# Kernel optimization log

Hardware: AMD Instinct MI355X
Metric: run time of the kernel (lower is better)

## Reference

```python
import jax, jax.numpy as jnp
import numpy as np

N = 4096          # n_neurons
M = 10            # max_memory
T = 10            # max_ticks
B = 1024          # batch
P = N // 2 // 2   # n_pairs = 1024
AD = 64           # attention_dim


def ln(x, g, b, eps=1e-5):
    m = x.mean(-1, keepdims=True)
    v = ((x - m) ** 2).mean(-1, keepdims=True)
    return (x - m) * jax.lax.rsqrt(v + eps) * g + b


def setup_inputs() -> dict:
    key = jax.random.key(0)
    ks = iter(jax.random.split(key, 64))

    def rn(shape, s=0.05):
        return (jax.random.normal(next(ks), shape) * s).astype(jnp.float32)

    d = {}
    d['x'] = jax.random.normal(next(ks), (B, 1, 28, 28), dtype=jnp.float32)
    d['post0'] = jax.random.normal(next(ks), (N, M), dtype=jnp.float32)
    d['pre0'] = jax.random.normal(next(ks), (N, M), dtype=jnp.float32)
    d['pairs'] = jax.random.randint(next(ks), (P, 2), 0, N)
    d['decay'] = jnp.full((P,), 0.1, jnp.float32)
    # image encoder: 784 -> 128 -> 32 -> 4
    d['ie_w1'] = rn((784, 128)); d['ie_b1'] = jnp.zeros(128); d['ie_g1'] = jnp.ones(128); d['ie_be1'] = jnp.zeros(128)
    d['ie_w2'] = rn((128, 32));  d['ie_b2'] = jnp.zeros(32);  d['ie_g2'] = jnp.ones(32);  d['ie_be2'] = jnp.zeros(32)
    d['ie_w3'] = rn((32, 4));    d['ie_b3'] = jnp.zeros(4)
    # synapse model: (4+N) -> 256 -> N
    d['sy_w1'] = rn((4 + N, 256)); d['sy_b1'] = jnp.zeros(256); d['sy_g'] = jnp.ones(256); d['sy_be'] = jnp.zeros(256)
    d['sy_w2'] = rn((256, N));     d['sy_b2'] = jnp.zeros(N)
    # batched per-neuron models: M -> 128 -> 1
    d['nm_w1'] = rn((N, M, 128)); d['nm_b1'] = jnp.zeros((N, 128))
    d['nm_g'] = jnp.ones((N, 128)); d['nm_be'] = jnp.zeros((N, 128))
    d['nm_w2'] = rn((N, 128));    d['nm_b2'] = jnp.zeros(N)
    # attention projections
    d['key_w'] = rn((4, AD)); d['key_b'] = jnp.zeros(AD)
    d['val_w'] = rn((4, AD)); d['val_b'] = jnp.zeros(AD)
    d['q_w'] = rn((P, AD));   d['q_b'] = jnp.zeros(AD)
    # syncronization reader: (AD+P) -> 512 -> 64 -> 10
    d['rd_w1'] = rn((AD + P, 512)); d['rd_b1'] = jnp.zeros(512); d['rd_g1'] = jnp.ones(512); d['rd_be1'] = jnp.zeros(512)
    d['rd_w2'] = rn((512, 64));     d['rd_b2'] = jnp.zeros(64);  d['rd_g2'] = jnp.ones(64);  d['rd_be2'] = jnp.zeros(64)
    d['rd_w3'] = rn((64, 10));      d['rd_b3'] = jnp.zeros(10)
    return d


def reference(x, post0, pre0, pairs, decay,
              ie_w1, ie_b1, ie_g1, ie_be1, ie_w2, ie_b2, ie_g2, ie_be2, ie_w3, ie_b3,
              sy_w1, sy_b1, sy_g, sy_be, sy_w2, sy_b2,
              nm_w1, nm_b1, nm_g, nm_be, nm_w2, nm_b2,
              key_w, key_b, val_w, val_b, q_w, q_b,
              rd_w1, rd_b1, rd_g1, rd_be1, rd_w2, rd_b2, rd_g2, rd_be2, rd_w3, rd_b3):
    b = x.shape[0]
    fx = x.reshape(b, -1)
    # image encoder
    e = jax.nn.relu(ln(fx @ ie_w1 + ie_b1, ie_g1, ie_be1))
    e = jax.nn.relu(ln(e @ ie_w2 + ie_b2, ie_g2, ie_be2))
    enc = e @ ie_w3 + ie_b3                               # [B,4]
    keys = enc @ key_w + key_b                            # [B,AD]
    values = enc @ val_w + val_b                          # [B,AD]
    post, pre = post0, pre0
    pred = None
    for tick in range(T):
        last_post = jnp.broadcast_to(post[:, -1][None, :], (b, N))
        syn_in = jnp.concatenate([enc, last_post], axis=1)            # [B,4+N]
        h = jax.nn.relu(ln(syn_in @ sy_w1 + sy_b1, sy_g, sy_be))
        new_pre = h @ sy_w2 + sy_b2                                   # [B,N]
        pre = jnp.concatenate([pre[:, 1:], new_pre.mean(0)[:, None]], axis=1)
        # batched per-neuron MLP over history
        h2 = jax.nn.relu(ln(jnp.einsum('nm,nmh->nh', pre, nm_w1) + nm_b1, nm_g, nm_be))
        new_post = jnp.einsum('nh,nh->n', h2, nm_w2) + nm_b2          # [N]
        post = jnp.concatenate([post[:, 1:], new_post[:, None]], axis=1)
        # decayed pair synchronization
        L = min(tick + 1, M)
        Zi = post[pairs[:, 0], M - L:]                                # [P,L]
        Zj = post[pairs[:, 1], M - L:]
        td = jnp.arange(L - 1, -1, -1, dtype=post.dtype)              # [L]
        R = jnp.exp(-decay[:, None] * td[None, :])                    # [P,L]
        sync = jnp.sum(Zi * R * Zj, axis=1) / (jnp.sum(R, axis=1) + 1e-8)  # [P]
        sv = jnp.broadcast_to(sync[None, :], (b, P))                  # [B,P]
        q = sv @ q_w + q_b                                            # [B,AD]
        scores = jnp.sum(q * keys, axis=-1, keepdims=True) / jnp.sqrt(jnp.float32(AD))
        aw = jax.nn.softmax(scores, axis=-1)                          # [B,1] -> ones
        att = aw * values                                             # [B,AD]
        comb = jnp.concatenate([att, sv], axis=-1)                    # [B,AD+P]
        r = jax.nn.relu(ln(comb @ rd_w1 + rd_b1, rd_g1, rd_be1))
        r = jax.nn.relu(ln(r @ rd_w2 + rd_b2, rd_g2, rd_be2))
        pred = r @ rd_w3 + rd_b3                                      # [B,10]
    return pred
```

## Files before the change

### kernel.cpp

```cpp
#include <hip/hip_runtime.h>

#define N_ 4096
#define M_ 10
#define T_ 10
#define B_ 1024
#define P_ 1024
#define NBLK 256
#define NTHR 512

__device__ __forceinline__ float wave_red_sum(float v) {
#pragma unroll
  for (int m = 32; m >= 1; m >>= 1) v += __shfl_xor(v, m);
  return v;
}

__device__ __forceinline__ float gld(const float* p) {
  return __hip_atomic_load(p, __ATOMIC_RELAXED, __HIP_MEMORY_SCOPE_AGENT);
}
__device__ __forceinline__ void gst(float* p, float v) {
  __hip_atomic_store(p, v, __ATOMIC_RELAXED, __HIP_MEMORY_SCOPE_AGENT);
}

__device__ __forceinline__ void gridbar(unsigned* bar, unsigned bar_no, int g) {
  asm volatile("s_waitcnt vmcnt(0)" ::: "memory");
  __syncthreads();
  if (threadIdx.x == 0) {
    __hip_atomic_fetch_add(&bar[(g & 7) * 32], 1u, __ATOMIC_RELAXED, __HIP_MEMORY_SCOPE_AGENT);
    if (g == 0) {
      const unsigned target = bar_no * (NBLK / 8);
      bool done;
      do {
        done = true;
#pragma unroll
        for (int i = 0; i < 8; ++i)
          done &= (__hip_atomic_load(&bar[i * 32], __ATOMIC_RELAXED, __HIP_MEMORY_SCOPE_AGENT) >= target);
        if (!done) __builtin_amdgcn_s_sleep(1);
      } while (!done);
#pragma unroll
      for (int i = 0; i < 8; ++i)
        __hip_atomic_store(&bar[256 + i * 32], bar_no, __ATOMIC_RELAXED, __HIP_MEMORY_SCOPE_AGENT);
    } else {
      unsigned* mygen = &bar[256 + (g & 7) * 32];
      while (__hip_atomic_load(mygen, __ATOMIC_RELAXED, __HIP_MEMORY_SCOPE_AGENT) < bar_no)
        __builtin_amdgcn_s_sleep(1);
    }
  }
  asm volatile("" ::: "memory");
  __syncthreads();
}

__global__ void k_init(unsigned* __restrict__ bar) {
  if (threadIdx.x < 512)
    __hip_atomic_store(bar + threadIdx.x, 0u, __ATOMIC_RELAXED, __HIP_MEMORY_SCOPE_AGENT);
}

struct MArgs {
  const float *x, *post0, *pre0;
  const int* pairs;
  const float* decay;
  const float *iew1, *ieb1, *ieg1, *iebe1, *iew2, *ieb2, *ieg2, *iebe2, *iew3, *ieb3;
  const float *syw1, *syb1, *syg, *sybe, *syw2, *syb2;
  const float *nw1, *nb1, *ng, *nbe, *nw2, *nb2;
  const float *vw, *vb;
  const float *rdw1, *rdb1, *rdg1, *rdbe1, *rdw2, *rdb2, *rdg2, *rdbe2, *rdw3, *rdb3;
  float *pc, *pc2, *enc_g, *hbar, *postG, *syncv, *scp;
  float* out;
  unsigned* bar;
};

__global__ __launch_bounds__(NTHR)
void k_mega(MArgs a) {
  const int g = blockIdx.x, tid = threadIdx.x;
  const int lane = tid & 63;
  const int n0 = g * 16;
  const int b0e = g * 4;

  __shared__ float s_w1[16 * M_ * 128];
  __shared__ float s_syw1[16 * 256];
  __shared__ float s_w4[4 * 256];
  __shared__ float scratch[6144];
  __shared__ float s_post[16][M_];
  __shared__ float s_pre[16][M_];
  __shared__ float s_pl[16];
  __shared__ float s_hbar[256];
  __shared__ float s_cval[256];
  __shared__ float s_tmp[2][256];
  __shared__ float s_red[16];
  __shared__ float s_values[4][64];
  __shared__ float s_stat[6];
  __shared__ float s_mw[4];
  __shared__ float s_mww[16];

  unsigned bar_no = 0;

  {
    const float4* src = (const float4*)(a.nw1 + n0 * M_ * 128);
    float4* dst = (float4*)s_w1;
    for (int i = tid; i < 16 * M_ * 128 / 4; i += NTHR) dst[i] = src[i];
    const float4* s2 = (const float4*)(a.syw1 + (4 + n0) * 256);
    float4* d2 = (float4*)s_syw1;
    for (int i = tid; i < 16 * 256 / 4; i += NTHR) d2[i] = s2[i];
    const float4* s3 = (const float4*)a.syw1;
    float4* d3 = (float4*)s_w4;
    for (int i = tid; i < 1024 / 4; i += NTHR) d3[i] = s3[i];
    if (tid < 160) {
      int r = tid / 10, m = tid - r * 10;
      s_post[r][m] = a.post0[(n0 + r) * M_ + m];
      s_pre[r][m]  = a.pre0[(n0 + r) * M_ + m];
    }
    float* fx = scratch;
    for (int i = tid; i < 4 * 784; i += NTHR) fx[i] = a.x[b0e * 784 + i];
  }
  __syncthreads();
  if (tid < 16) s_pl[tid] = s_post[tid][M_ - 1];

  {
    float* fx = scratch;
    float* e1 = scratch + 3200;
    int r = tid >> 7, j = tid & 127;
    float u = a.ieb1[j];
    const float* fxr = fx + r * 784;
    for (int k = 0; k < 784; ++k) u += fxr[k] * a.iew1[k * 128 + j];
    float s = wave_red_sum(u), sq = wave_red_sum(u * u);
    int w = tid >> 6;
    if (lane == 0) { s_tmp[0][w] = s; s_tmp[1][w] = sq; }
    __syncthreads();
    float S = s_tmp[0][r * 2] + s_tmp[0][r * 2 + 1];
    float S2 = s_tmp[1][r * 2] + s_tmp[1][r * 2 + 1];
    float mm = S * (1.f / 128.f), vv = S2 * (1.f / 128.f) - mm * mm;
    e1[r * 128 + j] = fmaxf((u - mm) * rsqrtf(vv + 1e-5f) * a.ieg1[j] + a.iebe1[j], 0.f);
  }
  __syncthreads();
  {
    float* e1 = scratch + 3200;
    float* e2 = scratch + 3712;
    if (tid < 128) {
      int r = tid >> 5, jj = tid & 31;
      float u = a.ieb2[jj];
      for (int k = 0; k < 128; ++k) u += e1[r * 128 + k] * a.iew2[k * 32 + jj];
      float ss = u, sq = u * u;
#pragma unroll
      for (int m = 16; m >= 1; m >>= 1) { ss += __shfl_xor(ss, m, 32); sq += __shfl_xor(sq, m, 32); }
      float mm = ss * (1.f / 32.f), vv = sq * (1.f / 32.f) - mm * mm;
      e2[r * 32 + jj] = fmaxf((u - mm) * rsqrtf(vv + 1e-5f) * a.ieg2[jj] + a.iebe2[jj], 0.f);
    }
  }
  __syncthreads();
  {
    float* e2 = scratch + 3712;
    float* encs = scratch + 3840;
    if (tid < 16) {
      int r = tid >> 2, o = tid & 3;
      float u = a.ieb3[o];
      for (int k = 0; k < 32; ++k) u += e2[r * 32 + k] * a.iew3[k * 4 + o];
      encs[r * 4 + o] = u;
      gst(&a.enc_g[(b0e + r) * 4 + o], u);
    }
    __syncthreads();
    if (tid < 256) {
      int r = tid >> 6, v = tid & 63;
      float u = a.vb[v];
#pragma unroll
      for (int o = 0; o < 4; ++o) u += encs[r * 4 + o] * a.vw[o * 64 + v];
      s_values[r][v] = u;
    }
  }
  __syncthreads();
  {
    int j = tid & 255, half = tid >> 8;
    float acc = 0.f;
#pragma unroll
    for (int r = 0; r < 8; ++r) {
      int n = half * 8 + r;
      acc += s_pl[n] * s_syw1[n * 256 + j];
    }
    s_tmp[half][j] = acc;
  }
  __syncthreads();
  if (tid < 256) gst(&a.pc[g * 256 + tid], s_tmp[0][tid] + s_tmp[1][tid]);
  ++bar_no; gridbar(a.bar, bar_no, g);

  for (int t = 0; t < T_; ++t) {
    if (g < 8) {
      int j = tid & 255, half = tid >> 8;
      float acc = 0.f;
#pragma unroll 4
      for (int r = 0; r < 16; ++r)
        acc += gld(&a.pc[(g * 32 + half * 16 + r) * 256 + j]);
      s_tmp[half][j] = acc;
      __syncthreads();
      if (tid < 256) gst(&a.pc2[g * 256 + tid], s_tmp[0][tid] + s_tmp[1][tid]);
    }
    ++bar_no; gridbar(a.bar, bar_no, g);

    if (g < 64) {
      float* encT = scratch;
      float* mb = scratch + 4096;
      float* rb = scratch + 5120;
      if (t == 0) {
        for (int i = tid; i < 4096; i += NTHR) {
          int b = i >> 2, o = i & 3;
          encT[o * 1024 + b] = gld(&a.enc_g[i]);
        }
        float q[14];
        if (tid < 256) {
          float w0 = s_w4[tid], w1v = s_w4[256 + tid], w2v = s_w4[512 + tid], w3v = s_w4[768 + tid];
          float wv[4] = {w0, w1v, w2v, w3v};
          int idx = 0;
#pragma unroll
          for (int o = 0; o < 4; ++o) q[idx++] = wv[o];
#pragma unroll
          for (int o = 0; o < 4; ++o)
#pragma unroll
            for (int p = 0; p <= o; ++p) q[idx++] = wv[o] * wv[p];
        } else {
#pragma unroll
          for (int i = 0; i < 14; ++i) q[i] = 0.f;
        }
#pragma unroll
        for (int i = 0; i < 14; ++i) q[i] = wave_red_sum(q[i]);
        if (lane == 0) {
          int w = tid >> 6;
#pragma unroll
          for (int i = 0; i < 14; ++i) s_tmp[1][w * 16 + i] = q[i];
        }
        __syncthreads();
        if (tid < 14) {
          float S = 0.f;
#pragma unroll
          for (int w = 0; w < 8; ++w) S += s_tmp[1][w * 16 + tid];
          s_red[tid] = S * (1.f / 256.f);
        }
        __syncthreads();
        if (tid < 4) s_mw[tid] = s_red[tid];
        if (tid < 16) {
          int o = tid >> 2, p = tid & 3;
          int hi = o > p ? o : p, lo = o > p ? p : o;
          s_mww[tid] = s_red[4 + hi * (hi + 1) / 2 + lo];
        }
        __syncthreads();
      }
      if (tid < 256) {
        float acc = a.syb1[tid];
#pragma unroll
        for (int s = 0; s < 8; ++s) acc += gld(&a.pc2[s * 256 + tid]);
        s_cval[tid] = acc;
      }
      __syncthreads();
      {
        float p[6];
        if (tid < 256) {
          float c = s_cval[tid];
          p[0] = c; p[1] = c * c;
          p[2] = c * s_w4[tid];
          p[3] = c * s_w4[256 + tid];
          p[4] = c * s_w4[512 + tid];
          p[5] = c * s_w4[768 + tid];
        } else {
#pragma unroll
          for (int i = 0; i < 6; ++i) p[i] = 0.f;
        }
#pragma unroll
        for (int i = 0; i < 6; ++i) p[i] = wave_red_sum(p[i]);
        if (lane == 0) {
          int w = tid >> 6;
#pragma unroll
          for (int i = 0; i < 6; ++i) s_tmp[0][w * 8 + i] = p[i];
        }
        __syncthreads();
        if (tid < 6) {
          float S = 0.f;
#pragma unroll
          for (int w = 0; w < 8; ++w) S += s_tmp[0][w * 8 + tid];
          s_stat[tid] = S * (1.f / 256.f);
        }
        __syncthreads();
      }
      for (int b = tid; b < 1024; b += NTHR) {
        float e0 = encT[b], e1v = encT[1024 + b], e2v = encT[2048 + b], e3v = encT[3072 + b];
        float m = s_stat[0] + e0 * s_mw[0] + e1v * s_mw[1] + e2v * s_mw[2] + e3v * s_mw[3];
        float eu2 = s_stat[1] + 2.f * (e0 * s_stat[2] + e1v * s_stat[3] + e2v * s_stat[4] + e3v * s_stat[5]);
        float ee[4] = {e0, e1v, e2v, e3v};
        float qf = 0.f;
#pragma unroll
        for (int o = 0; o < 4; ++o)
#pragma unroll
          for (int p = 0; p < 4; ++p) qf += ee[o] * ee[p] * s_mww[o * 4 + p];
        eu2 += qf;
        mb[b] = m;
        rb[b] = rsqrtf(eu2 - m * m + 1e-5f);
      }
      __syncthreads();
      {
        int jj = 4 * g + (tid >> 7);
        int bt = tid & 127;
        float cj = s_cval[jj];
        float w0 = s_w4[jj], w1v = s_w4[256 + jj], w2v = s_w4[512 + jj], w3v = s_w4[768 + jj];
        float gj = a.syg[jj], bj = a.sybe[jj];
        float acc = 0.f;
#pragma unroll
        for (int bb = 0; bb < 8; ++bb) {
          int b = bb * 128 + bt;
          float u = cj + encT[b] * w0 + encT[1024 + b] * w1v + encT[2048 + b] * w2v + encT[3072 + b] * w3v;
          float y = (u - mb[b]) * rb[b] * gj + bj;
          acc += fmaxf(y, 0.f);
        }
        acc = wave_red_sum(acc);
        int w = tid >> 6;
        if (lane == 0) s_tmp[0][w] = acc;
        __syncthreads();
        if ((tid & 127) == 0)
          gst(&a.hbar[jj], (s_tmp[0][w] + s_tmp[0][w + 1]) * (1.f / 1024.f));
      }
    }
    ++bar_no; gridbar(a.bar, bar_no, g);

    {
      if (tid < 256) s_hbar[tid] = gld(&a.hbar[tid]);
      __syncthreads();
      {
        int nl = tid & 15, kq = tid >> 4;
        float u = 0.f;
#pragma unroll
        for (int kk = 0; kk < 8; ++kk) {
          int k = kq * 8 + kk;
          u += s_hbar[k] * a.syw2[k * N_ + n0 + nl];
        }
        ((float*)s_tmp)[kq * 16 + nl] = u;
      }
      __syncthreads();
      if (tid < 16) {
        float v = a.syb2[n0 + tid];
#pragma unroll
        for (int q = 0; q < 32; ++q) v += ((float*)s_tmp)[q * 16 + tid];
#pragma unroll
        for (int m = 0; m < M_ - 1; ++m) s_pre[tid][m] = s_pre[tid][m + 1];
        s_pre[tid][M_ - 1] = v;
      }
      __syncthreads();
      {
        int grp = tid >> 7, jj = tid & 127;
        int wv = tid >> 6;
#pragma unroll
        for (int rd = 0; rd < 4; ++rd) {
          int nl = rd * 4 + grp;
          int n2 = n0 + nl;
          float u = a.nb1[n2 * 128 + jj];
#pragma unroll
          for (int m = 0; m < M_; ++m) u += s_pre[nl][m] * s_w1[(nl * M_ + m) * 128 + jj];
          float s = wave_red_sum(u), sq = wave_red_sum(u * u);
          if (lane == 0) { s_red[wv * 2] = s; s_red[wv * 2 + 1] = sq; }
          __syncthreads();
          float S = s_red[grp * 4 + 0] + s_red[grp * 4 + 2];
          float S2 = s_red[grp * 4 + 1] + s_red[grp * 4 + 3];
          float mm = S * (1.f / 128.f), vv = S2 * (1.f / 128.f) - mm * mm;
          float y = fmaxf((u - mm) * rsqrtf(vv + 1e-5f) * a.ng[n2 * 128 + jj] + a.nbe[n2 * 128 + jj], 0.f);
          float d = wave_red_sum(y * a.nw2[n2 * 128 + jj]);
          __syncthreads();
          if (lane == 0) s_red[wv] = d;
          __syncthreads();
          if (jj == 0) {
            float npost = s_red[grp * 2] + s_red[grp * 2 + 1] + a.nb2[n2];
#pragma unroll
            for (int m = 0; m < M_ - 1; ++m) s_post[nl][m] = s_post[nl][m + 1];
            s_post[nl][M_ - 1] = npost;
            s_pl[nl] = npost;
          }
          __syncthreads();
        }
      }
      if (t < T_ - 1) {
        int j = tid & 255, half = tid >> 8;
        float acc = 0.f;
#pragma unroll
        for (int r = 0; r < 8; ++r) {
          int n = half * 8 + r;
          acc += s_pl[n] * s_syw1[n * 256 + j];
        }
        s_tmp[half][j] = acc;
        __syncthreads();
        if (tid < 256) gst(&a.pc[g * 256 + tid], s_tmp[0][tid] + s_tmp[1][tid]);
      } else {
        if (tid < 160) {
          int r = tid / 10, m = tid - r * 10;
          gst(&a.postG[(n0 + r) * M_ + m], s_post[r][m]);
        }
      }
    }
    ++bar_no; gridbar(a.bar, bar_no, g);
  }

  if (tid < 4) {
    int p = g * 4 + tid;
    int i = a.pairs[p * 2], jn = a.pairs[p * 2 + 1];
    float dc = a.decay[p];
    float num = 0.f, den = 0.f;
#pragma unroll
    for (int l = 0; l < M_; ++l) {
      float r = expf(-dc * (float)(M_ - 1 - l));
      num += gld(&a.postG[i * M_ + l]) * r * gld(&a.postG[jn * M_ + l]);
      den += r;
    }
    gst(&a.syncv[p], num / (den + 1e-8f));
  }
  ++bar_no; gridbar(a.bar, bar_no, g);

  if (g < 8) {
    if (tid < 128) s_tmp[0][tid] = gld(&a.syncv[g * 128 + tid]);
    __syncthreads();
    float acc = 0.f;
    for (int i = 0; i < 128; ++i)
      acc += s_tmp[0][i] * a.rdw1[(64 + g * 128 + i) * 512 + tid];
    gst(&a.scp[g * 512 + tid], acc);
  }
  ++bar_no; gridbar(a.bar, bar_no, g);

  {
    float* r1 = scratch;
    float* r2 = scratch + 2048;
    float* red = scratch + 2304;
    float* p2 = scratch + 2368;
    float base = a.rdb1[tid];
#pragma unroll
    for (int s = 0; s < 8; ++s) base += gld(&a.scp[s * 512 + tid]);
    float u[4];
#pragma unroll
    for (int r = 0; r < 4; ++r) u[r] = base;
    for (int k = 0; k < 64; ++k) {
      float w = a.rdw1[k * 512 + tid];
#pragma unroll
      for (int r = 0; r < 4; ++r) u[r] += s_values[r][k] * w;
    }
    int wid = tid >> 6;
#pragma unroll
    for (int r = 0; r < 4; ++r) {
      float s = wave_red_sum(u[r]), sq = wave_red_sum(u[r] * u[r]);
      if (lane == 0) { red[r * 16 + wid * 2] = s; red[r * 16 + wid * 2 + 1] = sq; }
    }
    __syncthreads();
    float gg = a.rdg1[tid], bb = a.rdbe1[tid];
#pragma unroll
    for (int r = 0; r < 4; ++r) {
      float S = 0.f, S2 = 0.f;
#pragma unroll
      for (int w = 0; w < 8; ++w) { S += red[r * 16 + w * 2]; S2 += red[r * 16 + w * 2 + 1]; }
      float m = S * (1.f / 512.f), v = S2 * (1.f / 512.f) - m * m;
      r1[r * 512 + tid] = fmaxf((u[r] - m) * rsqrtf(v + 1e-5f) * gg + bb, 0.f);
    }
    __syncthreads();
    int o = tid & 63, kq = tid >> 6;
    float u2[4] = {0.f, 0.f, 0.f, 0.f};
#pragma unroll
    for (int kk = 0; kk < 64; ++kk) {
      int k = kq * 64 + kk;
      float w = a.rdw2[k * 64 + o];
#pragma unroll
      for (int r = 0; r < 4; ++r) u2[r] += r1[r * 512 + k] * w;
    }
#pragma unroll
    for (int r = 0; r < 4; ++r) p2[(kq * 4 + r) * 64 + o] = u2[r];
    __syncthreads();
    if (tid < 256) {
      int r = tid >> 6, o2 = tid & 63;
      float v = a.rdb2[o2];
#pragma unroll
      for (int q = 0; q < 8; ++q) v += p2[(q * 4 + r) * 64 + o2];
      float s = wave_red_sum(v), sq = wave_red_sum(v * v);
      float m = s * (1.f / 64.f), var = sq * (1.f / 64.f) - m * m;
      r2[r * 64 + o2] = fmaxf((v - m) * rsqrtf(var + 1e-5f) * a.rdg2[o2] + a.rdbe2[o2], 0.f);
    }
    __syncthreads();
    if (tid < 40) {
      int r = tid / 10, o3 = tid - r * 10;
      float acc = a.rdb3[o3];
#pragma unroll
      for (int k = 0; k < 64; ++k) acc += r2[r * 64 + k] * a.rdw3[k * 10 + o3];
      a.out[(b0e + r) * 10 + o3] = acc;
    }
  }
}

extern "C" void kernel_launch(void* const* d_in, const int* in_sizes, int n_in,
                              void* d_out, int out_size, void* d_ws, size_t ws_size,
                              hipStream_t stream) {
  MArgs a;
  a.x     = (const float*)d_in[0];
  a.post0 = (const float*)d_in[1];
  a.pre0  = (const float*)d_in[2];
  a.pairs = (const int*)d_in[3];
  a.decay = (const float*)d_in[4];
  a.iew1  = (const float*)d_in[5];
  a.ieb1  = (const float*)d_in[6];
  a.ieg1  = (const float*)d_in[7];
  a.iebe1 = (const float*)d_in[8];
  a.iew2  = (const float*)d_in[9];
  a.ieb2  = (const float*)d_in[10];
  a.ieg2  = (const float*)d_in[11];
  a.iebe2 = (const float*)d_in[12];
  a.iew3  = (const float*)d_in[13];
  a.ieb3  = (const float*)d_in[14];
  a.syw1  = (const float*)d_in[15];
  a.syb1  = (const float*)d_in[16];
  a.syg   = (const float*)d_in[17];
  a.sybe  = (const float*)d_in[18];
  a.syw2  = (const float*)d_in[19];
  a.syb2  = (const float*)d_in[20];
  a.nw1   = (const float*)d_in[21];
  a.nb1   = (const float*)d_in[22];
  a.ng    = (const float*)d_in[23];
  a.nbe   = (const float*)d_in[24];
  a.nw2   = (const float*)d_in[25];
  a.nb2   = (const float*)d_in[26];
  a.vw    = (const float*)d_in[29];
  a.vb    = (const float*)d_in[30];
  a.rdw1  = (const float*)d_in[33];
  a.rdb1  = (const float*)d_in[34];
  a.rdg1  = (const float*)d_in[35];
  a.rdbe1 = (const float*)d_in[36];
  a.rdw2  = (const float*)d_in[37];
  a.rdb2  = (const float*)d_in[38];
  a.rdg2  = (const float*)d_in[39];
  a.rdbe2 = (const float*)d_in[40];
  a.rdw3  = (const float*)d_in[41];
  a.rdb3  = (const float*)d_in[42];
  a.out = (float*)d_out;

  float* ws = (float*)d_ws;
  a.pc    = ws;
  a.pc2   = ws + 65536;
  a.enc_g = ws + 67584;
  a.hbar  = ws + 71680;
  a.postG = ws + 71936;
  a.syncv = ws + 112896;
  a.scp   = ws + 113920;
  a.bar   = (unsigned*)(ws + 118016);

  k_init<<<1, 512, 0, stream>>>(a.bar);
  k_mega<<<NBLK, NTHR, 0, stream>>>(a);
}
```

Before: 212.5 us.

## Replace grid barriers with targeted counters and flags between producer/consumer block subsets

Replaces the full grid barrier (one master block polling, then broadcasting) with monotonic arrival counters and flags. Each stage now waits only for the blocks that produce its inputs: 8 reducer blocks wait on all 256, block 0 waits on the reducers, 64 blocks wait on block 0's flag, and everyone waits on those 64. Block 0 now computes the shared column statistics once and publishes them, instead of all 64 blocks recomputing them. The per-neuron MLP loop is also restructured to process 16 neurons in parallel with 32-lane shuffles instead of 4 serial rounds with block syncs. The cost is more intricate ordering logic and an extra serialized hop through block 0.

```diff
diff --git a/kernel.cpp b/kernel.cpp
--- a/kernel.cpp
+++ b/kernel.cpp
@@ -20,37 +20,39 @@
 __device__ __forceinline__ void gst(float* p, float v) {
   __hip_atomic_store(p, v, __ATOMIC_RELAXED, __HIP_MEMORY_SCOPE_AGENT);
 }
-
-__device__ __forceinline__ void gridbar(unsigned* bar, unsigned bar_no, int g) {
+__device__ __forceinline__ unsigned ld_u(unsigned* p) {
+  return __hip_atomic_load(p, __ATOMIC_RELAXED, __HIP_MEMORY_SCOPE_AGENT);
+}
+
+__device__ __forceinline__ void drain_sync() {
   asm volatile("s_waitcnt vmcnt(0)" ::: "memory");
   __syncthreads();
+}
+__device__ __forceinline__ void arrive8(unsigned* line8, int g) {
+  if (threadIdx.x == 0)
+    __hip_atomic_fetch_add(&line8[(g & 7) * 32], 1u, __ATOMIC_RELAXED, __HIP_MEMORY_SCOPE_AGENT);
+}
+__device__ __forceinline__ void wait_sum8(unsigned* line8, unsigned target) {
   if (threadIdx.x == 0) {
-    __hip_atomic_fetch_add(&bar[(g & 7) * 32], 1u, __ATOMIC_RELAXED, __HIP_MEMORY_SCOPE_AGENT);
-    if (g == 0) {
-      const unsigned target = bar_no * (NBLK / 8);
-      bool done;
-      do {
-        done = true;
-#pragma unroll
-        for (int i = 0; i < 8; ++i)
-          done &= (__hip_atomic_load(&bar[i * 32], __ATOMIC_RELAXED, __HIP_MEMORY_SCOPE_AGENT) >= target);
-        if (!done) __builtin_amdgcn_s_sleep(1);
-      } while (!done);
-#pragma unroll
-      for (int i = 0; i < 8; ++i)
-        __hip_atomic_store(&bar[256 + i * 32], bar_no, __ATOMIC_RELAXED, __HIP_MEMORY_SCOPE_AGENT);
-    } else {
-      unsigned* mygen = &bar[256 + (g & 7) * 32];
-      while (__hip_atomic_load(mygen, __ATOMIC_RELAXED, __HIP_MEMORY_SCOPE_AGENT) < bar_no)
-        __builtin_amdgcn_s_sleep(1);
-    }
-  }
-  asm volatile("" ::: "memory");
+    unsigned s;
+    do {
+      s = 0;
+#pragma unroll
+      for (int i = 0; i < 8; ++i) s += ld_u(&line8[i * 32]);
+      if (s < target) __builtin_amdgcn_s_sleep(1);
+    } while (s < target);
+  }
+  __syncthreads();
+}
+__device__ __forceinline__ void wait_word(unsigned* f, unsigned target) {
+  if (threadIdx.x == 0) {
+    while (ld_u(f) < target) __builtin_amdgcn_s_sleep(1);
+  }
   __syncthreads();
 }
 
 __global__ void k_init(unsigned* __restrict__ bar) {
-  if (threadIdx.x < 512)
+  if (threadIdx.x < 1024)
     __hip_atomic_store(bar + threadIdx.x, 0u, __ATOMIC_RELAXED, __HIP_MEMORY_SCOPE_AGENT);
 }
 
@@ -63,7 +65,7 @@
   const float *nw1, *nb1, *ng, *nbe, *nw2, *nb2;
   const float *vw, *vb;
   const float *rdw1, *rdb1, *rdg1, *rdbe1, *rdw2, *rdb2, *rdg2, *rdbe2, *rdw3, *rdb3;
-  float *pc, *pc2, *enc_g, *hbar, *postG, *syncv, *scp;
+  float *pc, *pc2, *enc_g, *hbar, *postG, *syncv, *scp, *cstat;
   float* out;
   unsigned* bar;
 };
@@ -72,26 +74,28 @@
 void k_mega(MArgs a) {
   const int g = blockIdx.x, tid = threadIdx.x;
   const int lane = tid & 63;
-  const int n0 = g * 16;
-  const int b0e = g * 4;
+  const int n0 = g * 16, b0e = g * 4;
 
   __shared__ float s_w1[16 * M_ * 128];
   __shared__ float s_syw1[16 * 256];
   __shared__ float s_w4[4 * 256];
-  __shared__ float scratch[6144];
+  __shared__ float reg1[4096];
+  __shared__ float reg2[1024];
+  __shared__ float s_mbrb[2048];
+  __shared__ float s_values[4][64];
   __shared__ float s_post[16][M_];
   __shared__ float s_pre[16][M_];
   __shared__ float s_pl[16];
   __shared__ float s_hbar[256];
-  __shared__ float s_cval[256];
   __shared__ float s_tmp[2][256];
   __shared__ float s_red[16];
-  __shared__ float s_values[4][64];
-  __shared__ float s_stat[6];
-  __shared__ float s_mw[4];
-  __shared__ float s_mww[16];
-
-  unsigned bar_no = 0;
+  __shared__ float s_stats[20];
+  __shared__ float s_static[14];
+
+  unsigned* barA = a.bar;
+  unsigned* barC = a.bar + 256;
+  unsigned* barR = a.bar + 512;
+  unsigned* flagB = a.bar + 544;
 
   {
     const float4* src = (const float4*)(a.nw1 + n0 * M_ * 128);
@@ -108,18 +112,15 @@
       s_post[r][m] = a.post0[(n0 + r) * M_ + m];
       s_pre[r][m]  = a.pre0[(n0 + r) * M_ + m];
     }
-    float* fx = scratch;
-    for (int i = tid; i < 4 * 784; i += NTHR) fx[i] = a.x[b0e * 784 + i];
+    for (int i = tid; i < 4 * 784; i += NTHR) reg1[i] = a.x[b0e * 784 + i];
   }
   __syncthreads();
   if (tid < 16) s_pl[tid] = s_post[tid][M_ - 1];
 
   {
-    float* fx = scratch;
-    float* e1 = scratch + 3200;
     int r = tid >> 7, j = tid & 127;
     float u = a.ieb1[j];
-    const float* fxr = fx + r * 784;
+    const float* fxr = reg1 + r * 784;
     for (int k = 0; k < 784; ++k) u += fxr[k] * a.iew1[k * 128 + j];
     float s = wave_red_sum(u), sq = wave_red_sum(u * u);
     int w = tid >> 6;
@@ -128,42 +129,34 @@
     float S = s_tmp[0][r * 2] + s_tmp[0][r * 2 + 1];
     float S2 = s_tmp[1][r * 2] + s_tmp[1][r * 2 + 1];
     float mm = S * (1.f / 128.f), vv = S2 * (1.f / 128.f) - mm * mm;
-    e1[r * 128 + j] = fmaxf((u - mm) * rsqrtf(vv + 1e-5f) * a.ieg1[j] + a.iebe1[j], 0.f);
-  }
-  __syncthreads();
-  {
-    float* e1 = scratch + 3200;
-    float* e2 = scratch + 3712;
-    if (tid < 128) {
-      int r = tid >> 5, jj = tid & 31;
-      float u = a.ieb2[jj];
-      for (int k = 0; k < 128; ++k) u += e1[r * 128 + k] * a.iew2[k * 32 + jj];
-      float ss = u, sq = u * u;
-#pragma unroll
-      for (int m = 16; m >= 1; m >>= 1) { ss += __shfl_xor(ss, m, 32); sq += __shfl_xor(sq, m, 32); }
-      float mm = ss * (1.f / 32.f), vv = sq * (1.f / 32.f) - mm * mm;
-      e2[r * 32 + jj] = fmaxf((u - mm) * rsqrtf(vv + 1e-5f) * a.ieg2[jj] + a.iebe2[jj], 0.f);
-    }
-  }
-  __syncthreads();
-  {
-    float* e2 = scratch + 3712;
-    float* encs = scratch + 3840;
-    if (tid < 16) {
-      int r = tid >> 2, o = tid & 3;
-      float u = a.ieb3[o];
-      for (int k = 0; k < 32; ++k) u += e2[r * 32 + k] * a.iew3[k * 4 + o];
-      encs[r * 4 + o] = u;
-      gst(&a.enc_g[(b0e + r) * 4 + o], u);
-    }
-    __syncthreads();
-    if (tid < 256) {
-      int r = tid >> 6, v = tid & 63;
-      float u = a.vb[v];
-#pragma unroll
-      for (int o = 0; o < 4; ++o) u += encs[r * 4 + o] * a.vw[o * 64 + v];
-      s_values[r][v] = u;
-    }
+    reg2[r * 128 + j] = fmaxf((u - mm) * rsqrtf(vv + 1e-5f) * a.ieg1[j] + a.iebe1[j], 0.f);
+  }
+  __syncthreads();
+  if (tid < 128) {
+    int r = tid >> 5, jj = tid & 31;
+    float u = a.ieb2[jj];
+    for (int k = 0; k < 128; ++k) u += reg2[r * 128 + k] * a.iew2[k * 32 + jj];
+    float ss = u, sq = u * u;
+#pragma unroll
+    for (int m = 16; m >= 1; m >>= 1) { ss += __shfl_xor(ss, m, 32); sq += __shfl_xor(sq, m, 32); }
+    float mm = ss * (1.f / 32.f), vv = sq * (1.f / 32.f) - mm * mm;
+    reg2[512 + r * 32 + jj] = fmaxf((u - mm) * rsqrtf(vv + 1e-5f) * a.ieg2[jj] + a.iebe2[jj], 0.f);
+  }
+  __syncthreads();
+  if (tid < 16) {
+    int r = tid >> 2, o = tid & 3;
+    float u = a.ieb3[o];
+    for (int k = 0; k < 32; ++k) u += reg2[512 + r * 32 + k] * a.iew3[k * 4 + o];
+    reg2[640 + r * 4 + o] = u;
+    gst(&a.enc_g[(b0e + r) * 4 + o], u);
+  }
+  __syncthreads();
+  if (tid < 256) {
+    int r = tid >> 6, v = tid & 63;
+    float u = a.vb[v];
+#pragma unroll
+    for (int o = 0; o < 4; ++o) u += reg2[640 + r * 4 + o] * a.vw[o * 64 + v];
+    s_values[r][v] = u;
   }
   __syncthreads();
   {
@@ -178,218 +171,227 @@
   }
   __syncthreads();
   if (tid < 256) gst(&a.pc[g * 256 + tid], s_tmp[0][tid] + s_tmp[1][tid]);
-  ++bar_no; gridbar(a.bar, bar_no, g);
+  drain_sync();
+  arrive8(barA, g);
 
   for (int t = 0; t < T_; ++t) {
     if (g < 8) {
+      wait_sum8(barA, 256u * (unsigned)(t + 1));
       int j = tid & 255, half = tid >> 8;
       float acc = 0.f;
-#pragma unroll 4
+#pragma unroll
       for (int r = 0; r < 16; ++r)
         acc += gld(&a.pc[(g * 32 + half * 16 + r) * 256 + j]);
       s_tmp[half][j] = acc;
       __syncthreads();
       if (tid < 256) gst(&a.pc2[g * 256 + tid], s_tmp[0][tid] + s_tmp[1][tid]);
-    }
-    ++bar_no; gridbar(a.bar, bar_no, g);
-
+      drain_sync();
+      if (tid == 0)
+        __hip_atomic_fetch_add(barR, 1u, __ATOMIC_RELAXED, __HIP_MEMORY_SCOPE_AGENT);
+    }
+    if (g == 0) {
+      wait_word(barR, 8u * (unsigned)(t + 1));
+      float cv = 0.f;
+      if (tid < 256) {
+        cv = a.syb1[tid];
+#pragma unroll
+        for (int s = 0; s < 8; ++s) cv += gld(&a.pc2[s * 256 + tid]);
+      }
+      if (t == 0) {
+        float q[14];
+        if (tid < 256) {
+          float wv[4] = {s_w4[tid], s_w4[256 + tid], s_w4[512 + tid], s_w4[768 + tid]};
+          int idx = 0;
+#pragma unroll
+          for (int o = 0; o < 4; ++o) q[idx++] = wv[o];
+#pragma unroll
+          for (int o = 0; o < 4; ++o)
+#pragma unroll
+            for (int p = 0; p <= o; ++p) q[idx++] = wv[o] * wv[p];
+        } else {
+#pragma unroll
+          for (int i = 0; i < 14; ++i) q[i] = 0.f;
+        }
+#pragma unroll
+        for (int i = 0; i < 14; ++i) q[i] = wave_red_sum(q[i]);
+        int w = tid >> 6;
+        if (lane == 0) {
+#pragma unroll
+          for (int i = 0; i < 14; ++i) s_tmp[1][w * 16 + i] = q[i];
+        }
+        __syncthreads();
+        if (tid < 14) {
+          float S = 0.f;
+#pragma unroll
+          for (int w2 = 0; w2 < 8; ++w2) S += s_tmp[1][w2 * 16 + tid];
+          s_static[tid] = S * (1.f / 256.f);
+        }
+        __syncthreads();
+      }
+      {
+        float p[6];
+        if (tid < 256) {
+          p[0] = cv; p[1] = cv * cv;
+          p[2] = cv * s_w4[tid]; p[3] = cv * s_w4[256 + tid];
+          p[4] = cv * s_w4[512 + tid]; p[5] = cv * s_w4[768 + tid];
+        } else {
+#pragma unroll
+          for (int i = 0; i < 6; ++i) p[i] = 0.f;
+        }
+#pragma unroll
+        for (int i = 0; i < 6; ++i) p[i] = wave_red_sum(p[i]);
+        int w = tid >> 6;
+        if (lane == 0) {
+#pragma unroll
+          for (int i = 0; i < 6; ++i) s_tmp[0][w * 8 + i] = p[i];
+        }
+        __syncthreads();
+        if (tid < 6) {
+          float S = 0.f;
+#pragma unroll
+          for (int w2 = 0; w2 < 8; ++w2) S += s_tmp[0][w2 * 8 + tid];
+          gst(&a.cstat[256 + tid], S * (1.f / 256.f));
+        }
+      }
+      if (tid < 256) gst(&a.cstat[tid], cv);
+      if (tid < 14) gst(&a.cstat[262 + tid], s_static[tid]);
+      drain_sync();
+      if (tid == 0)
+        __hip_atomic_store(flagB, (unsigned)(t + 1), __ATOMIC_RELAXED, __HIP_MEMORY_SCOPE_AGENT);
+    }
     if (g < 64) {
-      float* encT = scratch;
-      float* mb = scratch + 4096;
-      float* rb = scratch + 5120;
+      wait_word(flagB, (unsigned)(t + 1));
       if (t == 0) {
         for (int i = tid; i < 4096; i += NTHR) {
           int b = i >> 2, o = i & 3;
-          encT[o * 1024 + b] = gld(&a.enc_g[i]);
-        }
-        float q[14];
-        if (tid < 256) {
-          float w0 = s_w4[tid], w1v = s_w4[256 + tid], w2v = s_w4[512 + tid], w3v = s_w4[768 + tid];
-          float wv[4] = {w0, w1v, w2v, w3v};
-          int idx = 0;
-#pragma unroll
-          for (int o = 0; o < 4; ++o) q[idx++] = wv[o];
-#pragma unroll
-          for (int o = 0; o < 4; ++o)
-#pragma unroll
-            for (int p = 0; p <= o; ++p) q[idx++] = wv[o] * wv[p];
-        } else {
-#pragma unroll
-          for (int i = 0; i < 14; ++i) q[i] = 0.f;
-        }
-#pragma unroll
-        for (int i = 0; i < 14; ++i) q[i] = wave_red_sum(q[i]);
-        if (lane == 0) {
-          int w = tid >> 6;
-#pragma unroll
-          for (int i = 0; i < 14; ++i) s_tmp[1][w * 16 + i] = q[i];
-        }
-        __syncthreads();
-        if (tid < 14) {
-          float S = 0.f;
-#pragma unroll
-          for (int w = 0; w < 8; ++w) S += s_tmp[1][w * 16 + tid];
-          s_red[tid] = S * (1.f / 256.f);
-        }
-        __syncthreads();
-        if (tid < 4) s_mw[tid] = s_red[tid];
-        if (tid < 16) {
-          int o = tid >> 2, p = tid & 3;
-          int hi = o > p ? o : p, lo = o > p ? p : o;
-          s_mww[tid] = s_red[4 + hi * (hi + 1) / 2 + lo];
-        }
-        __syncthreads();
-      }
-      if (tid < 256) {
-        float acc = a.syb1[tid];
-#pragma unroll
-        for (int s = 0; s < 8; ++s) acc += gld(&a.pc2[s * 256 + tid]);
-        s_cval[tid] = acc;
+          reg1[o * 1024 + b] = gld(&a.enc_g[i]);
+        }
+      }
+      if (tid < 20) s_stats[tid] = gld(&a.cstat[256 + tid]);
+      if (tid < 4)  s_red[tid] = gld(&a.cstat[4 * g + tid]);
+      __syncthreads();
+      for (int b = tid; b < 1024; b += NTHR) {
+        float e0 = reg1[b], e1v = reg1[1024 + b], e2v = reg1[2048 + b], e3v = reg1[3072 + b];
+        float m = s_stats[0] + e0 * s_stats[6] + e1v * s_stats[7] + e2v * s_stats[8] + e3v * s_stats[9];
+        float eu2 = s_stats[1] + 2.f * (e0 * s_stats[2] + e1v * s_stats[3] + e2v * s_stats[4] + e3v * s_stats[5]);
+        float qf = e0 * e0 * s_stats[10]
+                 + 2.f * e1v * e0 * s_stats[11] + e1v * e1v * s_stats[12]
+                 + 2.f * e2v * e0 * s_stats[13] + 2.f * e2v * e1v * s_stats[14] + e2v * e2v * s_stats[15]
+                 + 2.f * e3v * e0 * s_stats[16] + 2.f * e3v * e1v * s_stats[17]
+                 + 2.f * e3v * e2v * s_stats[18] + e3v * e3v * s_stats[19];
+        eu2 += qf;
+        s_mbrb[b] = m;
+        s_mbrb[1024 + b] = rsqrtf(eu2 - m * m + 1e-5f);
       }
       __syncthreads();
       {
-        float p[6];
-        if (tid < 256) {
-          float c = s_cval[tid];
-          p[0] = c; p[1] = c * c;
-          p[2] = c * s_w4[tid];
-          p[3] = c * s_w4[256 + tid];
-          p[4] = c * s_w4[512 + tid];
-          p[5] = c * s_w4[768 + tid];
-        } else {
-#pragma unroll
-          for (int i = 0; i < 6; ++i) p[i] = 0.f;
-        }
-#pragma unroll
-        for (int i = 0; i < 6; ++i) p[i] = wave_red_sum(p[i]);
-        if (lane == 0) {
-          int w = tid >> 6;
-#pragma unroll
-          for (int i = 0; i < 6; ++i) s_tmp[0][w * 8 + i] = p[i];
-        }
-        __syncthreads();
-        if (tid < 6) {
-          float S = 0.f;
-#pragma unroll
-          for (int w = 0; w < 8; ++w) S += s_tmp[0][w * 8 + tid];
-          s_stat[tid] = S * (1.f / 256.f);
-        }
-        __syncthreads();
-      }
-      for (int b = tid; b < 1024; b += NTHR) {
-        float e0 = encT[b], e1v = encT[1024 + b], e2v = encT[2048 + b], e3v = encT[3072 + b];
-        float m = s_stat[0] + e0 * s_mw[0] + e1v * s_mw[1] + e2v * s_mw[2] + e3v * s_mw[3];
-        float eu2 = s_stat[1] + 2.f * (e0 * s_stat[2] + e1v * s_stat[3] + e2v * s_stat[4] + e3v * s_stat[5]);
-        float ee[4] = {e0, e1v, e2v, e3v};
-        float qf = 0.f;
-#pragma unroll
-        for (int o = 0; o < 4; ++o)
-#pragma unroll
-          for (int p = 0; p < 4; ++p) qf += ee[o] * ee[p] * s_mww[o * 4 + p];
-        eu2 += qf;
-        mb[b] = m;
-        rb[b] = rsqrtf(eu2 - m * m + 1e-5f);
-      }
-      __syncthreads();
-      {
-        int jj = 4 * g + (tid >> 7);
-        int bt = tid & 127;
-        float cj = s_cval[jj];
+        int q = tid >> 7, bt = tid & 127;
+        int jj = 4 * g + q;
+        float cj = s_red[q];
         float w0 = s_w4[jj], w1v = s_w4[256 + jj], w2v = s_w4[512 + jj], w3v = s_w4[768 + jj];
         float gj = a.syg[jj], bj = a.sybe[jj];
         float acc = 0.f;
 #pragma unroll
         for (int bb = 0; bb < 8; ++bb) {
           int b = bb * 128 + bt;
-          float u = cj + encT[b] * w0 + encT[1024 + b] * w1v + encT[2048 + b] * w2v + encT[3072 + b] * w3v;
-          float y = (u - mb[b]) * rb[b] * gj + bj;
+          float u = cj + reg1[b] * w0 + reg1[1024 + b] * w1v + reg1[2048 + b] * w2v + reg1[3072 + b] * w3v;
+          float y = (u - s_mbrb[b]) * s_mbrb[1024 + b] * gj + bj;
           acc += fmaxf(y, 0.f);
         }
         acc = wave_red_sum(acc);
-        int w = tid >> 6;
-        if (lane == 0) s_tmp[0][w] = acc;
+        int wv = tid >> 6;
+        if (lane == 0) s_tmp[0][wv] = acc;
         __syncthreads();
         if ((tid & 127) == 0)
-          gst(&a.hbar[jj], (s_tmp[0][w] + s_tmp[0][w + 1]) * (1.f / 1024.f));
-      }
-    }
-    ++bar_no; gridbar(a.bar, bar_no, g);
-
+          gst(&a.hbar[jj], (s_tmp[0][wv] + s_tmp[0][wv + 1]) * (1.f / 1024.f));
+      }
+      drain_sync();
+      arrive8(barC, g);
+    }
+    wait_sum8(barC, 64u * (unsigned)(t + 1));
+    if (tid < 256) s_hbar[tid] = gld(&a.hbar[tid]);
+    __syncthreads();
     {
-      if (tid < 256) s_hbar[tid] = gld(&a.hbar[tid]);
+      int nl = tid & 15, kq = tid >> 4;
+      float u = 0.f;
+#pragma unroll
+      for (int kk = 0; kk < 8; ++kk) {
+        int k = kq * 8 + kk;
+        u += s_hbar[k] * a.syw2[k * N_ + n0 + nl];
+      }
+      ((float*)s_tmp)[kq * 16 + nl] = u;
+    }
+    __syncthreads();
+    if (tid < 16) {
+      float v = a.syb2[n0 + tid];
+#pragma unroll
+      for (int q2 = 0; q2 < 32; ++q2) v += ((float*)s_tmp)[q2 * 16 + tid];
+#pragma unroll
+      for (int m = 0; m < M_ - 1; ++m) s_pre[tid][m] = s_pre[tid][m + 1];
+      s_pre[tid][M_ - 1] = v;
+    }
+    __syncthreads();
+    {
+      int nl = tid >> 5, q = tid & 31;
+      int n2 = n0 + nl;
+      float pr[M_];
+#pragma unroll
+      for (int m = 0; m < M_; ++m) pr[m] = s_pre[nl][m];
+      float u[4];
+#pragma unroll
+      for (int k = 0; k < 4; ++k) {
+        int j = q + 32 * k;
+        float uu = a.nb1[n2 * 128 + j];
+#pragma unroll
+        for (int m = 0; m < M_; ++m) uu += pr[m] * s_w1[(nl * M_ + m) * 128 + j];
+        u[k] = uu;
+      }
+      float s = u[0] + u[1] + u[2] + u[3];
+      float sq = u[0] * u[0] + u[1] * u[1] + u[2] * u[2] + u[3] * u[3];
+#pragma unroll
+      for (int m = 16; m >= 1; m >>= 1) { s += __shfl_xor(s, m, 32); sq += __shfl_xor(sq, m, 32); }
+      float mm = s * (1.f / 128.f), vv = sq * (1.f / 128.f) - mm * mm;
+      float ri = rsqrtf(vv + 1e-5f);
+      float d = 0.f;
+#pragma unroll
+      for (int k = 0; k < 4; ++k) {
+        int j = q + 32 * k;
+        float y = fmaxf((u[k] - mm) * ri * a.ng[n2 * 128 + j] + a.nbe[n2 * 128 + j], 0.f);
+        d += y * a.nw2[n2 * 128 + j];
+      }
+#pragma unroll
+      for (int m = 16; m >= 1; m >>= 1) d += __shfl_xor(d, m, 32);
+      if (q == 0) {
+        float npost = d + a.nb2[n2];
+#pragma unroll
+        for (int m = 0; m < M_ - 1; ++m) s_post[nl][m] = s_post[nl][m + 1];
+        s_post[nl][M_ - 1] = npost;
+        s_pl[nl] = npost;
+      }
+    }
+    __syncthreads();
+    if (t < T_ - 1) {
+      int j = tid & 255, half = tid >> 8;
+      float acc = 0.f;
+#pragma unroll
+      for (int r = 0; r < 8; ++r) {
+        int n = half * 8 + r;
+        acc += s_pl[n] * s_syw1[n * 256 + j];
+      }
+      s_tmp[half][j] = acc;
       __syncthreads();
-      {
-        int nl = tid & 15, kq = tid >> 4;
-        float u = 0.f;
-#pragma unroll
-        for (int kk = 0; kk < 8; ++kk) {
-          int k = kq * 8 + kk;
-          u += s_hbar[k] * a.syw2[k * N_ + n0 + nl];
-        }
-        ((float*)s_tmp)[kq * 16 + nl] = u;
-      }
-      __syncthreads();
-      if (tid < 16) {
-        float v = a.syb2[n0 + tid];
-#pragma unroll
-        for (int q = 0; q < 32; ++q) v += ((float*)s_tmp)[q * 16 + tid];
-#pragma unroll
-        for (int m = 0; m < M_ - 1; ++m) s_pre[tid][m] = s_pre[tid][m + 1];
-        s_pre[tid][M_ - 1] = v;
-      }
-      __syncthreads();
-      {
-        int grp = tid >> 7, jj = tid & 127;
-        int wv = tid >> 6;
-#pragma unroll
-        for (int rd = 0; rd < 4; ++rd) {
-          int nl = rd * 4 + grp;
-          int n2 = n0 + nl;
-          float u = a.nb1[n2 * 128 + jj];
-#pragma unroll
-          for (int m = 0; m < M_; ++m) u += s_pre[nl][m] * s_w1[(nl * M_ + m) * 128 + jj];
-          float s = wave_red_sum(u), sq = wave_red_sum(u * u);
-          if (lane == 0) { s_red[wv * 2] = s; s_red[wv * 2 + 1] = sq; }
-          __syncthreads();
-          float S = s_red[grp * 4 + 0] + s_red[grp * 4 + 2];
-          float S2 = s_red[grp * 4 + 1] + s_red[grp * 4 + 3];
-          float mm = S * (1.f / 128.f), vv = S2 * (1.f / 128.f) - mm * mm;
-          float y = fmaxf((u - mm) * rsqrtf(vv + 1e-5f) * a.ng[n2 * 128 + jj] + a.nbe[n2 * 128 + jj], 0.f);
-          float d = wave_red_sum(y * a.nw2[n2 * 128 + jj]);
-          __syncthreads();
-          if (lane == 0) s_red[wv] = d;
-          __syncthreads();
-          if (jj == 0) {
-            float npost = s_red[grp * 2] + s_red[grp * 2 + 1] + a.nb2[n2];
-#pragma unroll
-            for (int m = 0; m < M_ - 1; ++m) s_post[nl][m] = s_post[nl][m + 1];
-            s_post[nl][M_ - 1] = npost;
-            s_pl[nl] = npost;
-          }
-          __syncthreads();
-        }
-      }
-      if (t < T_ - 1) {
-        int j = tid & 255, half = tid >> 8;
-        float acc = 0.f;
-#pragma unroll
-        for (int r = 0; r < 8; ++r) {
-          int n = half * 8 + r;
-          acc += s_pl[n] * s_syw1[n * 256 + j];
-        }
-        s_tmp[half][j] = acc;
-        __syncthreads();
-        if (tid < 256) gst(&a.pc[g * 256 + tid], s_tmp[0][tid] + s_tmp[1][tid]);
-      } else {
-        if (tid < 160) {
-          int r = tid / 10, m = tid - r * 10;
-          gst(&a.postG[(n0 + r) * M_ + m], s_post[r][m]);
-        }
-      }
-    }
-    ++bar_no; gridbar(a.bar, bar_no, g);
-  }
-
+      if (tid < 256) gst(&a.pc[g * 256 + tid], s_tmp[0][tid] + s_tmp[1][tid]);
+    } else {
+      if (tid < 160) {
+        int r = tid / 10, m = tid - r * 10;
+        gst(&a.postG[(n0 + r) * M_ + m], s_post[r][m]);
+      }
+    }
+    drain_sync();
+    arrive8(barA, g);
+  }
+
+  wait_sum8(barA, 256u * 11u);
   if (tid < 4) {
     int p = g * 4 + tid;
     int i = a.pairs[p * 2], jn = a.pairs[p * 2 + 1];
@@ -403,23 +405,23 @@
     }
     gst(&a.syncv[p], num / (den + 1e-8f));
   }
-  ++bar_no; gridbar(a.bar, bar_no, g);
-
+  drain_sync();
+  arrive8(barA, g);
   if (g < 8) {
+    wait_sum8(barA, 256u * 12u);
     if (tid < 128) s_tmp[0][tid] = gld(&a.syncv[g * 128 + tid]);
     __syncthreads();
     float acc = 0.f;
     for (int i = 0; i < 128; ++i)
       acc += s_tmp[0][i] * a.rdw1[(64 + g * 128 + i) * 512 + tid];
     gst(&a.scp[g * 512 + tid], acc);
-  }
-  ++bar_no; gridbar(a.bar, bar_no, g);
-
+    drain_sync();
+    arrive8(barC, g);
+  }
+  wait_sum8(barC, 64u * 10u + 8u);
   {
-    float* r1 = scratch;
-    float* r2 = scratch + 2048;
-    float* red = scratch + 2304;
-    float* p2 = scratch + 2368;
+    float* r1 = reg1;
+    float* p2 = reg1 + 2048;
     float base = a.rdb1[tid];
 #pragma unroll
     for (int s = 0; s < 8; ++s) base += gld(&a.scp[s * 512 + tid]);
@@ -435,7 +437,7 @@
 #pragma unroll
     for (int r = 0; r < 4; ++r) {
       float s = wave_red_sum(u[r]), sq = wave_red_sum(u[r] * u[r]);
-      if (lane == 0) { red[r * 16 + wid * 2] = s; red[r * 16 + wid * 2 + 1] = sq; }
+      if (lane == 0) { s_tmp[0][r * 8 + wid] = s; s_tmp[1][r * 8 + wid] = sq; }
     }
     __syncthreads();
     float gg = a.rdg1[tid], bb = a.rdbe1[tid];
@@ -443,7 +445,7 @@
     for (int r = 0; r < 4; ++r) {
       float S = 0.f, S2 = 0.f;
 #pragma unroll
-      for (int w = 0; w < 8; ++w) { S += red[r * 16 + w * 2]; S2 += red[r * 16 + w * 2 + 1]; }
+      for (int w = 0; w < 8; ++w) { S += s_tmp[0][r * 8 + w]; S2 += s_tmp[1][r * 8 + w]; }
       float m = S * (1.f / 512.f), v = S2 * (1.f / 512.f) - m * m;
       r1[r * 512 + tid] = fmaxf((u[r] - m) * rsqrtf(v + 1e-5f) * gg + bb, 0.f);
     }
@@ -467,14 +469,14 @@
       for (int q = 0; q < 8; ++q) v += p2[(q * 4 + r) * 64 + o2];
       float s = wave_red_sum(v), sq = wave_red_sum(v * v);
       float m = s * (1.f / 64.f), var = sq * (1.f / 64.f) - m * m;
-      r2[r * 64 + o2] = fmaxf((v - m) * rsqrtf(var + 1e-5f) * a.rdg2[o2] + a.rdbe2[o2], 0.f);
+      reg2[r * 64 + o2] = fmaxf((v - m) * rsqrtf(var + 1e-5f) * a.rdg2[o2] + a.rdbe2[o2], 0.f);
     }
     __syncthreads();
     if (tid < 40) {
       int r = tid / 10, o3 = tid - r * 10;
       float acc = a.rdb3[o3];
 #pragma unroll
-      for (int k = 0; k < 64; ++k) acc += r2[r * 64 + k] * a.rdw3[k * 10 + o3];
+      for (int k = 0; k < 64; ++k) acc += reg2[r * 64 + k] * a.rdw3[k * 10 + o3];
       a.out[(b0e + r) * 10 + o3] = acc;
     }
   }
@@ -533,8 +535,9 @@
   a.postG = ws + 71936;
   a.syncv = ws + 112896;
   a.scp   = ws + 113920;
-  a.bar   = (unsigned*)(ws + 118016);
-
-  k_init<<<1, 512, 0, stream>>>(a.bar);
+  a.cstat = ws + 118016;
+  a.bar   = (unsigned*)(ws + 118528);
+
+  k_init<<<1, 1024, 0, stream>>>(a.bar);
   k_mega<<<NBLK, NTHR, 0, stream>>>(a);
 }
```

New measurement: 198.0 us. 6.8% less time.
